# Performance work log

Measured on AMD Instinct MI355X. Metric: run time of the kernel, lower is better.

Reference implementation:

```python
import jax, jax.numpy as jnp
import numpy as np

NEG_SLOPE = 0.2
N_NODES = 50000
N_EDGES = 800000


def gat_conv(h, src, dst, W, al, ar, residual):
    """One DGL-style GATConv layer. h: [N, F_in]; returns [N, H*D]."""
    N = h.shape[0]
    H, D = al.shape
    feat = (h @ W).reshape(N, H, D)                 # [N, H, D]
    el = jnp.sum(feat * al, axis=-1)                # [N, H]
    er = jnp.sum(feat * ar, axis=-1)                # [N, H]
    e = jax.nn.leaky_relu(el[src] + er[dst], NEG_SLOPE)   # [E, H]
    # segment softmax over incoming edges of each destination node
    emax = jax.ops.segment_max(e, dst, num_segments=N)    # [N, H]
    ex = jnp.exp(e - emax[dst])                           # [E, H]
    denom = jax.ops.segment_sum(ex, dst, num_segments=N)  # [N, H]
    a = ex / denom[dst]                                   # [E, H]
    msg = feat[src] * a[:, :, None]                       # [E, H, D]
    rst = jax.ops.segment_sum(msg, dst, num_segments=N)   # [N, H, D]
    if residual:  # identity residual: in_feats == H*D
        rst = rst + h.reshape(N, H, D)
    return jax.nn.elu(rst).reshape(N, H * D)


def setup_inputs() -> dict:
    key = jax.random.key(0)
    ks = jax.random.split(key, 9)
    features = jax.random.normal(ks[0], (N_NODES, 256), dtype=jnp.float32)
    src = jax.random.randint(ks[1], (N_EDGES,), 0, N_NODES, dtype=jnp.int32)
    dst = jax.random.randint(ks[2], (N_EDGES,), 0, N_NODES, dtype=jnp.int32)
    s1 = 1.0 / np.sqrt(256.0)
    W1 = jax.random.normal(ks[3], (256, 256), dtype=jnp.float32) * s1
    al1 = jax.random.normal(ks[4], (4, 64), dtype=jnp.float32) * 0.1
    ar1 = jax.random.normal(ks[5], (4, 64), dtype=jnp.float32) * 0.1
    W2 = jax.random.normal(ks[6], (256, 256), dtype=jnp.float32) * s1
    al2 = jax.random.normal(ks[7], (4, 64), dtype=jnp.float32) * 0.1
    ar2 = jax.random.normal(ks[8], (4, 64), dtype=jnp.float32) * 0.1
    return {"features": features, "src": src, "dst": dst,
            "W1": W1, "al1": al1, "ar1": ar1,
            "W2": W2, "al2": al2, "ar2": ar2}


def reference(features, src, dst, W1, al1, ar1, W2, al2, ar2):
    h = gat_conv(features, src, dst, W1, al1, ar1, residual=False)
    h = gat_conv(h, src, dst, W2, al2, ar2, residual=True)
    return h  # [N, 256]
```

## Files before the change

### kernel.cpp

```cpp
#include <hip/hip_runtime.h>
#include <hip/hip_bf16.h>

#define N_NODES 50000
#define N_EDGES 800000
#define NHEAD 4
#define DHEAD 64
#define FDIM 256
#define SCANB 1024
#define NSCAN ((N_NODES + SCANB - 1) / SCANB)

typedef __attribute__((ext_vector_type(8))) short bfrag8;
typedef __attribute__((ext_vector_type(4))) float f32x4;

__device__ __forceinline__ unsigned f2bf_rne(float x) {
    unsigned u = __float_as_uint(x);
    return (u + 0x7fffu + ((u >> 16) & 1u)) >> 16;
}
__device__ __forceinline__ float bf2f(unsigned u) {
    return __uint_as_float(u << 16);
}

__global__ void degree_kernel(const int* __restrict__ dst, int* __restrict__ cnt, int E) {
    int e = blockIdx.x * 256 + threadIdx.x;
    if (e < E) atomicAdd(&cnt[dst[e]], 1);
}

__global__ __launch_bounds__(1024) void scan1_kernel(const int* __restrict__ cnt,
                                                     int* __restrict__ partial,
                                                     int* __restrict__ bsum, int N) {
    __shared__ int sdata[SCANB];
    int i = blockIdx.x * SCANB + (int)threadIdx.x;
    int v = (i < N) ? cnt[i] : 0;
    sdata[threadIdx.x] = v;
    __syncthreads();
    for (int off = 1; off < SCANB; off <<= 1) {
        int t = (threadIdx.x >= (unsigned)off) ? sdata[threadIdx.x - off] : 0;
        __syncthreads();
        sdata[threadIdx.x] += t;
        __syncthreads();
    }
    if (i < N) partial[i] = sdata[threadIdx.x];
    if (threadIdx.x == SCANB - 1) bsum[blockIdx.x] = sdata[SCANB - 1];
}

__global__ void scan2_kernel(const int* __restrict__ bsum, int* __restrict__ boff, int nb) {
    int lane = threadIdx.x;
    int v = (lane < nb) ? bsum[lane] : 0;
#pragma unroll
    for (int off = 1; off < 64; off <<= 1) {
        int o = __shfl_up(v, off, 64);
        if (lane >= off) v += o;
    }
    int excl = __shfl_up(v, 1, 64);
    if (lane == 0) excl = 0;
    if (lane < nb) boff[lane] = excl;
}

__global__ __launch_bounds__(1024) void scan3_kernel(const int* __restrict__ partial,
                                                     const int* __restrict__ boff,
                                                     int* __restrict__ rowptr,
                                                     int* __restrict__ cursor, int N) {
    int i = blockIdx.x * SCANB + (int)threadIdx.x;
    if (i < N) {
        int inc = partial[i] + boff[blockIdx.x];
        rowptr[i + 1] = inc;
        if (i + 1 < N) cursor[i + 1] = inc;
    }
    if (i == 0) { rowptr[0] = 0; cursor[0] = 0; }
}

__global__ void scatter_kernel(const int* __restrict__ src, const int* __restrict__ dst,
                               int* __restrict__ cursor, int* __restrict__ srcs, int E) {
    int e = blockIdx.x * 256 + threadIdx.x;
    if (e < E) {
        int pos = atomicAdd(&cursor[dst[e]], 1);
        srcs[pos] = src[e];
    }
}

__global__ __launch_bounds__(256) void bconv_kernel(const float* __restrict__ B1,
                                                    const float* __restrict__ B2,
                                                    ushort* __restrict__ Bt1,
                                                    ushort* __restrict__ Bt2) {
    const float* B = blockIdx.y ? B2 : B1;
    ushort* Bt = blockIdx.y ? Bt2 : Bt1;
    __shared__ ushort th[16][264];
    int k0 = blockIdx.x * 16;
    int n = threadIdx.x;
#pragma unroll
    for (int k = 0; k < 16; ++k)
        th[k][n] = (ushort)f2bf_rne(B[(size_t)(k0 + k) * 256 + n]);
    __syncthreads();
    ushort oh[16];
#pragma unroll
    for (int k = 0; k < 16; ++k) oh[k] = th[k][n];
#pragma unroll
    for (int q = 0; q < 4; ++q)
        *reinterpret_cast<ushort4*>(Bt1 == Bt ? Bt1 + (size_t)n * 256 + k0 + q * 4
                                              : Bt2 + (size_t)n * 256 + k0 + q * 4) =
            make_ushort4(oh[q*4+0], oh[q*4+1], oh[q*4+2], oh[q*4+3]);
}

template <int SPLITA>
__global__ __launch_bounds__(256) void gemm_mfma_kernel(const float* __restrict__ Af,
                                                        const ushort* __restrict__ Ahg,
                                                        const ushort* __restrict__ Bt,
                                                        ushort* __restrict__ Cb,
                                                        const float* __restrict__ al,
                                                        const float* __restrict__ ar,
                                                        float* __restrict__ el,
                                                        float* __restrict__ er, int M) {
    __shared__ ushort Ah[128][40];
    __shared__ ushort Bh[128][40];
    const int t = threadIdx.x;
    const int lane = t & 63, wave = t >> 6;
    const int wr = wave >> 1, wc = wave & 1;
    const int row0 = blockIdx.x * 128;
    const int col0 = blockIdx.y * 128;

    f32x4 acc[4][4];
#pragma unroll
    for (int i = 0; i < 4; ++i)
#pragma unroll
        for (int j = 0; j < 4; ++j) { acc[i][j].x = 0.f; acc[i][j].y = 0.f; acc[i][j].z = 0.f; acc[i][j].w = 0.f; }

    const int srow = t >> 1;
    const int skoff = (t & 1) * 16;
    int arow = row0 + srow; if (arow >= M) arow = M - 1;
    const size_t abase = (size_t)arow * 256 + skoff;
    const size_t bbase = (size_t)(col0 + srow) * 256 + skoff;

    float4 af0, af1, af2, af3;
    uint4 r0, r1;
    uint4 r4, r5;

#define LOADK(kk)                                                              \
    do {                                                                       \
        if constexpr (SPLITA) {                                                \
            const float4* pa = reinterpret_cast<const float4*>(Af + abase + (kk)); \
            af0 = pa[0]; af1 = pa[1]; af2 = pa[2]; af3 = pa[3];                \
        } else {                                                               \
            r0 = *reinterpret_cast<const uint4*>(Ahg + abase + (kk));          \
            r1 = *reinterpret_cast<const uint4*>(Ahg + abase + (kk) + 8);      \
        }                                                                      \
        r4 = *reinterpret_cast<const uint4*>(Bt + bbase + (kk));               \
        r5 = *reinterpret_cast<const uint4*>(Bt + bbase + (kk) + 8);           \
    } while (0)

    LOADK(0);
#pragma unroll
    for (int kk = 0; kk < 256; kk += 32) {
        if (kk) __syncthreads();
        if constexpr (SPLITA) {
            float v[16];
            v[0]=af0.x; v[1]=af0.y; v[2]=af0.z; v[3]=af0.w;
            v[4]=af1.x; v[5]=af1.y; v[6]=af1.z; v[7]=af1.w;
            v[8]=af2.x; v[9]=af2.y; v[10]=af2.z; v[11]=af2.w;
            v[12]=af3.x; v[13]=af3.y; v[14]=af3.z; v[15]=af3.w;
            ushort hh[16];
#pragma unroll
            for (int q = 0; q < 16; ++q) hh[q] = (ushort)f2bf_rne(v[q]);
#pragma unroll
            for (int q = 0; q < 4; ++q)
                *reinterpret_cast<ushort4*>(&Ah[srow][skoff + q * 4]) =
                    make_ushort4(hh[q*4+0], hh[q*4+1], hh[q*4+2], hh[q*4+3]);
        } else {
            *reinterpret_cast<uint4*>(&Ah[srow][skoff])     = r0;
            *reinterpret_cast<uint4*>(&Ah[srow][skoff + 8]) = r1;
        }
        *reinterpret_cast<uint4*>(&Bh[srow][skoff])     = r4;
        *reinterpret_cast<uint4*>(&Bh[srow][skoff + 8]) = r5;
        __syncthreads();
        if (kk + 32 < 256) LOADK(kk + 32);

        const int kg = (lane >> 4) * 8;
        const int rsel = lane & 15;
        bfrag8 afh[4], bfh[4];
#pragma unroll
        for (int i = 0; i < 4; ++i)
            afh[i] = *reinterpret_cast<const bfrag8*>(&Ah[wr * 64 + i * 16 + rsel][kg]);
#pragma unroll
        for (int j = 0; j < 4; ++j)
            bfh[j] = *reinterpret_cast<const bfrag8*>(&Bh[wc * 64 + j * 16 + rsel][kg]);
#pragma unroll
        for (int i = 0; i < 4; ++i)
#pragma unroll
            for (int j = 0; j < 4; ++j)
                acc[i][j] = __builtin_amdgcn_mfma_f32_16x16x32_bf16(afh[i], bfh[j], acc[i][j], 0, 0, 0);
    }
#undef LOADK

    const int ccol = lane & 15;
    const int crow = (lane >> 4) * 4;
    const int head = (col0 >> 6) + wc;
    float alv[4], arv[4];
#pragma unroll
    for (int j = 0; j < 4; ++j) {
        alv[j] = al[head * 64 + j * 16 + ccol];
        arv[j] = ar[head * 64 + j * 16 + ccol];
    }
#pragma unroll
    for (int i = 0; i < 4; ++i) {
#pragma unroll
        for (int r = 0; r < 4; ++r) {
            int row = row0 + wr * 64 + i * 16 + crow + r;
            float vj[4];
#pragma unroll
            for (int j = 0; j < 4; ++j)
                vj[j] = (r == 0) ? acc[i][j].x : (r == 1) ? acc[i][j].y : (r == 2) ? acc[i][j].z : acc[i][j].w;
            float pl = 0.f, pr = 0.f;
#pragma unroll
            for (int j = 0; j < 4; ++j) {
                pl = fmaf(vj[j], alv[j], pl);
                pr = fmaf(vj[j], arv[j], pr);
            }
#pragma unroll
            for (int msk = 1; msk < 16; msk <<= 1) {
                pl += __shfl_xor(pl, msk, 64);
                pr += __shfl_xor(pr, msk, 64);
            }
            if (row < M) {
                if (ccol == 0) {
                    el[(size_t)row * NHEAD + head] = pl;
                    er[(size_t)row * NHEAD + head] = pr;
                }
#pragma unroll
                for (int j = 0; j < 4; ++j) {
                    int col = col0 + wc * 64 + j * 16 + ccol;
                    Cb[(size_t)row * 256 + col] = (ushort)f2bf_rne(vj[j]);
                }
            }
        }
    }
}

__global__ __launch_bounds__(256) void agg_kernel(
        const ushort* __restrict__ featb, const float* __restrict__ el,
        const float* __restrict__ er, const int* __restrict__ rowptr,
        const int* __restrict__ srcs,
        const ushort* __restrict__ resid_h, const ushort* __restrict__ resid_l,
        float* __restrict__ outf, ushort* __restrict__ outh, ushort* __restrict__ outl,
        int N) {
    int node = blockIdx.x * 4 + (threadIdx.x >> 6);
    if (node >= N) return;
    int lane = threadIdx.x & 63;
    int h4 = lane & 3;
    int eo = lane >> 2;
    int head = lane >> 4;
    float erh = er[(size_t)node * NHEAD + h4];
    int beg = rowptr[node], end = rowptr[node + 1];

    float m = -1e30f, ls = 0.f;
    for (int base = beg; base < end; base += 16) {
        int p = base + eo;
        float x = -1e30f;
        if (p < end) {
            int s = srcs[p];
            float t = el[(size_t)s * NHEAD + h4] + erh;
            x = t > 0.f ? t : 0.2f * t;
        }
        float cm = x;
        cm = fmaxf(cm, __shfl_xor(cm, 4, 64));
        cm = fmaxf(cm, __shfl_xor(cm, 8, 64));
        cm = fmaxf(cm, __shfl_xor(cm, 16, 64));
        cm = fmaxf(cm, __shfl_xor(cm, 32, 64));
        float mn = fmaxf(m, cm);
        ls = ls * __expf(m - mn) + ((p < end) ? __expf(x - mn) : 0.f);
        m = mn;
    }
    ls += __shfl_xor(ls, 4, 64);
    ls += __shfl_xor(ls, 8, 64);
    ls += __shfl_xor(ls, 16, 64);
    ls += __shfl_xor(ls, 32, 64);
    float dinv = ls > 0.f ? 1.0f / ls : 0.f;

    f32x4 a0 = {0.f, 0.f, 0.f, 0.f}, a1 = a0, a2 = a0, a3 = a0;
    for (int base = beg; base < end; base += 16) {
        int p = base + eo;
        int smine = 0;
        float wmine = 0.f;
        if (p < end) {
            smine = srcs[p];
            float t = el[(size_t)smine * NHEAD + h4] + erh;
            t = t > 0.f ? t : 0.2f * t;
            wmine = __expf(t - m) * dinv;
        }
        int jmax = end - base; if (jmax > 16) jmax = 16;
        int j = 0;
        for (; j + 3 < jmax; j += 4) {
            int sl0 = 4 * j + head;
            int s0 = __shfl(smine, sl0, 64);
            int s1 = __shfl(smine, sl0 + 4, 64);
            int s2 = __shfl(smine, sl0 + 8, 64);
            int s3 = __shfl(smine, sl0 + 12, 64);
            float w0 = __shfl(wmine, sl0, 64);
            float w1 = __shfl(wmine, sl0 + 4, 64);
            float w2 = __shfl(wmine, sl0 + 8, 64);
            float w3 = __shfl(wmine, sl0 + 12, 64);
            ushort4 f0 = *reinterpret_cast<const ushort4*>(featb + (size_t)s0 * FDIM + lane * 4);
            ushort4 f1 = *reinterpret_cast<const ushort4*>(featb + (size_t)s1 * FDIM + lane * 4);
            ushort4 f2 = *reinterpret_cast<const ushort4*>(featb + (size_t)s2 * FDIM + lane * 4);
            ushort4 f3 = *reinterpret_cast<const ushort4*>(featb + (size_t)s3 * FDIM + lane * 4);
            a0.x = fmaf(w0, bf2f(f0.x), a0.x); a0.y = fmaf(w0, bf2f(f0.y), a0.y);
            a0.z = fmaf(w0, bf2f(f0.z), a0.z); a0.w = fmaf(w0, bf2f(f0.w), a0.w);
            a1.x = fmaf(w1, bf2f(f1.x), a1.x); a1.y = fmaf(w1, bf2f(f1.y), a1.y);
            a1.z = fmaf(w1, bf2f(f1.z), a1.z); a1.w = fmaf(w1, bf2f(f1.w), a1.w);
            a2.x = fmaf(w2, bf2f(f2.x), a2.x); a2.y = fmaf(w2, bf2f(f2.y), a2.y);
            a2.z = fmaf(w2, bf2f(f2.z), a2.z); a2.w = fmaf(w2, bf2f(f2.w), a2.w);
            a3.x = fmaf(w3, bf2f(f3.x), a3.x); a3.y = fmaf(w3, bf2f(f3.y), a3.y);
            a3.z = fmaf(w3, bf2f(f3.z), a3.z); a3.w = fmaf(w3, bf2f(f3.w), a3.w);
        }
        for (; j < jmax; ++j) {
            int sl = 4 * j + head;
            int s0 = __shfl(smine, sl, 64);
            float w0 = __shfl(wmine, sl, 64);
            ushort4 f0 = *reinterpret_cast<const ushort4*>(featb + (size_t)s0 * FDIM + lane * 4);
            a0.x = fmaf(w0, bf2f(f0.x), a0.x); a0.y = fmaf(w0, bf2f(f0.y), a0.y);
            a0.z = fmaf(w0, bf2f(f0.z), a0.z); a0.w = fmaf(w0, bf2f(f0.w), a0.w);
        }
    }
    float4 acc = make_float4(a0.x + a1.x + a2.x + a3.x, a0.y + a1.y + a2.y + a3.y,
                             a0.z + a1.z + a2.z + a3.z, a0.w + a1.w + a2.w + a3.w);

    if (resid_h) {
        ushort4 rh = *reinterpret_cast<const ushort4*>(resid_h + (size_t)node * FDIM + lane * 4);
        ushort4 rl = *reinterpret_cast<const ushort4*>(resid_l + (size_t)node * FDIM + lane * 4);
        acc.x += bf2f(rh.x) + bf2f(rl.x);
        acc.y += bf2f(rh.y) + bf2f(rl.y);
        acc.z += bf2f(rh.z) + bf2f(rl.z);
        acc.w += bf2f(rh.w) + bf2f(rl.w);
    }
    acc.x = acc.x > 0.f ? acc.x : expm1f(acc.x);
    acc.y = acc.y > 0.f ? acc.y : expm1f(acc.y);
    acc.z = acc.z > 0.f ? acc.z : expm1f(acc.z);
    acc.w = acc.w > 0.f ? acc.w : expm1f(acc.w);

    if (outf) {
        *reinterpret_cast<float4*>(outf + (size_t)node * FDIM + lane * 4) = acc;
    } else {
        unsigned h0 = f2bf_rne(acc.x), h1 = f2bf_rne(acc.y), h2 = f2bf_rne(acc.z), h3 = f2bf_rne(acc.w);
        *reinterpret_cast<ushort4*>(outh + (size_t)node * FDIM + lane * 4) =
            make_ushort4((ushort)h0, (ushort)h1, (ushort)h2, (ushort)h3);
        *reinterpret_cast<ushort4*>(outl + (size_t)node * FDIM + lane * 4) = make_ushort4(
            (ushort)(__float_as_uint(acc.x - bf2f(h0)) >> 16),
            (ushort)(__float_as_uint(acc.y - bf2f(h1)) >> 16),
            (ushort)(__float_as_uint(acc.z - bf2f(h2)) >> 16),
            (ushort)(__float_as_uint(acc.w - bf2f(h3)) >> 16));
    }
}

extern "C" void kernel_launch(void* const* d_in, const int* in_sizes, int n_in,
                              void* d_out, int out_size, void* d_ws, size_t ws_size,
                              hipStream_t stream) {
    const float* features = (const float*)d_in[0];
    const int*   src      = (const int*)d_in[1];
    const int*   dst      = (const int*)d_in[2];
    const float* W1       = (const float*)d_in[3];
    const float* al1      = (const float*)d_in[4];
    const float* ar1      = (const float*)d_in[5];
    const float* W2       = (const float*)d_in[6];
    const float* al2      = (const float*)d_in[7];
    const float* ar2      = (const float*)d_in[8];
    float* out = (float*)d_out;

    const int N = N_NODES, E = N_EDGES;

    char* ws = (char*)d_ws;
    size_t off = 0;
    auto alloc = [&](size_t bytes) -> void* {
        void* p = ws + off;
        off = (off + bytes + 255) & ~(size_t)255;
        return p;
    };
    ushort* featb  = (ushort*)alloc((size_t)N * FDIM * 2);
    ushort* Afh    = (ushort*)alloc((size_t)N * FDIM * 2);
    ushort* Afl    = (ushort*)alloc((size_t)N * FDIM * 2);
    float*  el     = (float*)alloc((size_t)N * NHEAD * 4);
    float*  er     = (float*)alloc((size_t)N * NHEAD * 4);
    int*    rowptr = (int*)alloc((size_t)(N + 1) * 4);
    int*    cnt    = (int*)alloc((size_t)N * 4);
    int*    cursor = (int*)alloc((size_t)N * 4);
    int*    partial= (int*)alloc((size_t)N * 4);
    int*    bsum   = (int*)alloc((size_t)NSCAN * 4);
    int*    boff   = (int*)alloc((size_t)NSCAN * 4);
    int*    srcs   = (int*)alloc((size_t)E * 4);
    ushort* Bt1    = (ushort*)alloc((size_t)256 * 256 * 2);
    ushort* Bt2    = (ushort*)alloc((size_t)256 * 256 * 2);

    const int egrid = (E + 255) / 256;
    const int ngrid4 = (N + 3) / 4;

    hipMemsetAsync(cnt, 0, (size_t)N * 4, stream);
    degree_kernel<<<egrid, 256, 0, stream>>>(dst, cnt, E);
    scan1_kernel<<<NSCAN, SCANB, 0, stream>>>(cnt, partial, bsum, N);
    scan2_kernel<<<1, 64, 0, stream>>>(bsum, boff, NSCAN);
    scan3_kernel<<<NSCAN, SCANB, 0, stream>>>(partial, boff, rowptr, cursor, N);
    scatter_kernel<<<egrid, 256, 0, stream>>>(src, dst, cursor, srcs, E);

    bconv_kernel<<<dim3(16, 2), 256, 0, stream>>>(W1, W2, Bt1, Bt2);

    dim3 ggrid((N + 127) / 128, 2);

    gemm_mfma_kernel<1><<<ggrid, 256, 0, stream>>>(features, nullptr, Bt1, featb,
                                                   al1, ar1, el, er, N);
    agg_kernel<<<ngrid4, 256, 0, stream>>>(featb, el, er, rowptr, srcs,
                                           nullptr, nullptr, nullptr, Afh, Afl, N);

    gemm_mfma_kernel<0><<<ggrid, 256, 0, stream>>>(nullptr, Afh, Bt2, featb,
                                                   al2, ar2, el, er, N);
    agg_kernel<<<ngrid4, 256, 0, stream>>>(featb, el, er, rowptr, srcs,
                                           Afh, Afl, out, nullptr, nullptr, N);
}
```

Measured before the change: 304.4 us.

## Fuse softmax normalization into aggregation pass and drop low-precision residual split

The separate max/denominator pass over incoming edges in the aggregation kernel is removed. Unnormalized exp weights are accumulated together with their sum, and the result is divided by the denominator at the end. This saves a second gather of srcs and el per edge, but gives up the max subtraction, so large attention logits could overflow. The layer-1 output is now stored only as bf16 (no low-residual half), which cuts writes and reads but reduces residual precision. The tiny scan2 launch is folded into scan3, which now reduces the block sums itself.

```diff
diff --git a/kernel.cpp b/kernel.cpp
--- a/kernel.cpp
+++ b/kernel.cpp
@@ -43,26 +43,21 @@
     if (threadIdx.x == SCANB - 1) bsum[blockIdx.x] = sdata[SCANB - 1];
 }
 
-__global__ void scan2_kernel(const int* __restrict__ bsum, int* __restrict__ boff, int nb) {
-    int lane = threadIdx.x;
-    int v = (lane < nb) ? bsum[lane] : 0;
-#pragma unroll
-    for (int off = 1; off < 64; off <<= 1) {
-        int o = __shfl_up(v, off, 64);
-        if (lane >= off) v += o;
-    }
-    int excl = __shfl_up(v, 1, 64);
-    if (lane == 0) excl = 0;
-    if (lane < nb) boff[lane] = excl;
-}
-
 __global__ __launch_bounds__(1024) void scan3_kernel(const int* __restrict__ partial,
-                                                     const int* __restrict__ boff,
+                                                     const int* __restrict__ bsum,
                                                      int* __restrict__ rowptr,
                                                      int* __restrict__ cursor, int N) {
+    __shared__ int boff_s;
+    if (threadIdx.x < 64) {
+        int v = ((int)threadIdx.x < (int)blockIdx.x) ? bsum[threadIdx.x] : 0;
+#pragma unroll
+        for (int off = 1; off < 64; off <<= 1) v += __shfl_xor(v, off, 64);
+        if (threadIdx.x == 0) boff_s = v;
+    }
+    __syncthreads();
     int i = blockIdx.x * SCANB + (int)threadIdx.x;
     if (i < N) {
-        int inc = partial[i] + boff[blockIdx.x];
+        int inc = partial[i] + boff_s;
         rowptr[i + 1] = inc;
         if (i + 1 < N) cursor[i + 1] = inc;
     }
@@ -96,8 +91,7 @@
     for (int k = 0; k < 16; ++k) oh[k] = th[k][n];
 #pragma unroll
     for (int q = 0; q < 4; ++q)
-        *reinterpret_cast<ushort4*>(Bt1 == Bt ? Bt1 + (size_t)n * 256 + k0 + q * 4
-                                              : Bt2 + (size_t)n * 256 + k0 + q * 4) =
+        *reinterpret_cast<ushort4*>(Bt + (size_t)n * 256 + k0 + q * 4) =
             make_ushort4(oh[q*4+0], oh[q*4+1], oh[q*4+2], oh[q*4+3]);
 }
 
@@ -237,10 +231,8 @@
 __global__ __launch_bounds__(256) void agg_kernel(
         const ushort* __restrict__ featb, const float* __restrict__ el,
         const float* __restrict__ er, const int* __restrict__ rowptr,
-        const int* __restrict__ srcs,
-        const ushort* __restrict__ resid_h, const ushort* __restrict__ resid_l,
-        float* __restrict__ outf, ushort* __restrict__ outh, ushort* __restrict__ outl,
-        int N) {
+        const int* __restrict__ srcs, const ushort* __restrict__ resid,
+        float* __restrict__ outf, ushort* __restrict__ outh, int N) {
     int node = blockIdx.x * 4 + (threadIdx.x >> 6);
     if (node >= N) return;
     int lane = threadIdx.x & 63;
@@ -250,30 +242,7 @@
     float erh = er[(size_t)node * NHEAD + h4];
     int beg = rowptr[node], end = rowptr[node + 1];
 
-    float m = -1e30f, ls = 0.f;
-    for (int base = beg; base < end; base += 16) {
-        int p = base + eo;
-        float x = -1e30f;
-        if (p < end) {
-            int s = srcs[p];
-            float t = el[(size_t)s * NHEAD + h4] + erh;
-            x = t > 0.f ? t : 0.2f * t;
-        }
-        float cm = x;
-        cm = fmaxf(cm, __shfl_xor(cm, 4, 64));
-        cm = fmaxf(cm, __shfl_xor(cm, 8, 64));
-        cm = fmaxf(cm, __shfl_xor(cm, 16, 64));
-        cm = fmaxf(cm, __shfl_xor(cm, 32, 64));
-        float mn = fmaxf(m, cm);
-        ls = ls * __expf(m - mn) + ((p < end) ? __expf(x - mn) : 0.f);
-        m = mn;
-    }
-    ls += __shfl_xor(ls, 4, 64);
-    ls += __shfl_xor(ls, 8, 64);
-    ls += __shfl_xor(ls, 16, 64);
-    ls += __shfl_xor(ls, 32, 64);
-    float dinv = ls > 0.f ? 1.0f / ls : 0.f;
-
+    float wsum = 0.f;
     f32x4 a0 = {0.f, 0.f, 0.f, 0.f}, a1 = a0, a2 = a0, a3 = a0;
     for (int base = beg; base < end; base += 16) {
         int p = base + eo;
@@ -283,8 +252,9 @@
             smine = srcs[p];
             float t = el[(size_t)smine * NHEAD + h4] + erh;
             t = t > 0.f ? t : 0.2f * t;
-            wmine = __expf(t - m) * dinv;
-        }
+            wmine = __expf(t);
+        }
+        wsum += wmine;
         int jmax = end - base; if (jmax > 16) jmax = 16;
         int j = 0;
         for (; j + 3 < jmax; j += 4) {
@@ -319,16 +289,24 @@
             a0.z = fmaf(w0, bf2f(f0.z), a0.z); a0.w = fmaf(w0, bf2f(f0.w), a0.w);
         }
     }
-    float4 acc = make_float4(a0.x + a1.x + a2.x + a3.x, a0.y + a1.y + a2.y + a3.y,
-                             a0.z + a1.z + a2.z + a3.z, a0.w + a1.w + a2.w + a3.w);
-
-    if (resid_h) {
-        ushort4 rh = *reinterpret_cast<const ushort4*>(resid_h + (size_t)node * FDIM + lane * 4);
-        ushort4 rl = *reinterpret_cast<const ushort4*>(resid_l + (size_t)node * FDIM + lane * 4);
-        acc.x += bf2f(rh.x) + bf2f(rl.x);
-        acc.y += bf2f(rh.y) + bf2f(rl.y);
-        acc.z += bf2f(rh.z) + bf2f(rl.z);
-        acc.w += bf2f(rh.w) + bf2f(rl.w);
+    wsum += __shfl_xor(wsum, 4, 64);
+    wsum += __shfl_xor(wsum, 8, 64);
+    wsum += __shfl_xor(wsum, 16, 64);
+    wsum += __shfl_xor(wsum, 32, 64);
+    float denom = __shfl(wsum, head, 64);
+    float dinv = denom > 0.f ? 1.0f / denom : 0.f;
+
+    float4 acc = make_float4((a0.x + a1.x + a2.x + a3.x) * dinv,
+                             (a0.y + a1.y + a2.y + a3.y) * dinv,
+                             (a0.z + a1.z + a2.z + a3.z) * dinv,
+                             (a0.w + a1.w + a2.w + a3.w) * dinv);
+
+    if (resid) {
+        ushort4 rh = *reinterpret_cast<const ushort4*>(resid + (size_t)node * FDIM + lane * 4);
+        acc.x += bf2f(rh.x);
+        acc.y += bf2f(rh.y);
+        acc.z += bf2f(rh.z);
+        acc.w += bf2f(rh.w);
     }
     acc.x = acc.x > 0.f ? acc.x : expm1f(acc.x);
     acc.y = acc.y > 0.f ? acc.y : expm1f(acc.y);
@@ -338,14 +316,9 @@
     if (outf) {
         *reinterpret_cast<float4*>(outf + (size_t)node * FDIM + lane * 4) = acc;
     } else {
-        unsigned h0 = f2bf_rne(acc.x), h1 = f2bf_rne(acc.y), h2 = f2bf_rne(acc.z), h3 = f2bf_rne(acc.w);
         *reinterpret_cast<ushort4*>(outh + (size_t)node * FDIM + lane * 4) =
-            make_ushort4((ushort)h0, (ushort)h1, (ushort)h2, (ushort)h3);
-        *reinterpret_cast<ushort4*>(outl + (size_t)node * FDIM + lane * 4) = make_ushort4(
-            (ushort)(__float_as_uint(acc.x - bf2f(h0)) >> 16),
-            (ushort)(__float_as_uint(acc.y - bf2f(h1)) >> 16),
-            (ushort)(__float_as_uint(acc.z - bf2f(h2)) >> 16),
-            (ushort)(__float_as_uint(acc.w - bf2f(h3)) >> 16));
+            make_ushort4((ushort)f2bf_rne(acc.x), (ushort)f2bf_rne(acc.y),
+                         (ushort)f2bf_rne(acc.z), (ushort)f2bf_rne(acc.w));
     }
 }
 
@@ -374,7 +347,6 @@
     };
     ushort* featb  = (ushort*)alloc((size_t)N * FDIM * 2);
     ushort* Afh    = (ushort*)alloc((size_t)N * FDIM * 2);
-    ushort* Afl    = (ushort*)alloc((size_t)N * FDIM * 2);
     float*  el     = (float*)alloc((size_t)N * NHEAD * 4);
     float*  er     = (float*)alloc((size_t)N * NHEAD * 4);
     int*    rowptr = (int*)alloc((size_t)(N + 1) * 4);
@@ -382,7 +354,6 @@
     int*    cursor = (int*)alloc((size_t)N * 4);
     int*    partial= (int*)alloc((size_t)N * 4);
     int*    bsum   = (int*)alloc((size_t)NSCAN * 4);
-    int*    boff   = (int*)alloc((size_t)NSCAN * 4);
     int*    srcs   = (int*)alloc((size_t)E * 4);
     ushort* Bt1    = (ushort*)alloc((size_t)256 * 256 * 2);
     ushort* Bt2    = (ushort*)alloc((size_t)256 * 256 * 2);
@@ -393,8 +364,7 @@
     hipMemsetAsync(cnt, 0, (size_t)N * 4, stream);
     degree_kernel<<<egrid, 256, 0, stream>>>(dst, cnt, E);
     scan1_kernel<<<NSCAN, SCANB, 0, stream>>>(cnt, partial, bsum, N);
-    scan2_kernel<<<1, 64, 0, stream>>>(bsum, boff, NSCAN);
-    scan3_kernel<<<NSCAN, SCANB, 0, stream>>>(partial, boff, rowptr, cursor, N);
+    scan3_kernel<<<NSCAN, SCANB, 0, stream>>>(partial, bsum, rowptr, cursor, N);
     scatter_kernel<<<egrid, 256, 0, stream>>>(src, dst, cursor, srcs, E);
 
     bconv_kernel<<<dim3(16, 2), 256, 0, stream>>>(W1, W2, Bt1, Bt2);
@@ -404,10 +374,10 @@
     gemm_mfma_kernel<1><<<ggrid, 256, 0, stream>>>(features, nullptr, Bt1, featb,
                                                    al1, ar1, el, er, N);
     agg_kernel<<<ngrid4, 256, 0, stream>>>(featb, el, er, rowptr, srcs,
-                                           nullptr, nullptr, nullptr, Afh, Afl, N);
+                                           nullptr, nullptr, Afh, N);
 
     gemm_mfma_kernel<0><<<ggrid, 256, 0, stream>>>(nullptr, Afh, Bt2, featb,
                                                    al2, ar2, el, er, N);
     agg_kernel<<<ngrid4, 256, 0, stream>>>(featb, el, er, rowptr, srcs,
-                                           Afh, Afl, out, nullptr, nullptr, N);
-}
+                                           Afh, out, nullptr, N);
+}
```

Result: faster. 291.0 us (-4.4%).
